# Optimization experiments

Hardware: AMD Instinct MI355X
Metric: run time of the kernel (lower is better)

Reference implementation:

```python
import jax, jax.numpy as jnp
import numpy as np

N_NODES = 100000


def gcn_conv(x, W, b, src, dst, n):
    # PyG GCNConv: linear transform, add self-loops, symmetric degree normalization,
    # scatter-add aggregation from src -> dst, then bias.
    h = x @ W  # [N, F_out]
    loop = jnp.arange(n, dtype=src.dtype)
    s = jnp.concatenate([src, loop])  # sources incl. self-loops
    d = jnp.concatenate([dst, loop])  # targets incl. self-loops
    deg = jax.ops.segment_sum(jnp.ones_like(d, dtype=h.dtype), d, num_segments=n)
    dinv = jnp.where(deg > 0, jax.lax.rsqrt(deg), 0.0)
    norm = dinv[s] * dinv[d]  # [E+N]
    msg = h[s] * norm[:, None]  # gather + scale
    out = jax.ops.segment_sum(msg, d, num_segments=n)  # scatter-add
    return out + b


def setup_inputs() -> dict:
    key = jax.random.key(0)
    k1, k2, k3, k4 = jax.random.split(key, 4)
    n, e = N_NODES, 1600000
    z = jax.random.normal(k1, (n, 64), dtype=jnp.float32)
    edge_index = jax.random.randint(k2, (2, e), 0, n, dtype=jnp.int64)
    # Glorot-ish init for weights, zero bias (PyG default bias init is zeros)
    W1 = jax.random.normal(k3, (64, 128), dtype=jnp.float32) * (1.0 / np.sqrt(64))
    b1 = jnp.zeros((128,), dtype=jnp.float32)
    W2 = jax.random.normal(k4, (128, 64), dtype=jnp.float32) * (1.0 / np.sqrt(128))
    b2 = jnp.zeros((64,), dtype=jnp.float32)
    return {"z": z, "edge_index": edge_index, "W1": W1, "b1": b1, "W2": W2, "b2": b2}


def reference(z, edge_index, W1, b1, W2, b2):
    n = z.shape[0]
    src, dst = edge_index[0], edge_index[1]
    h = gcn_conv(z, W1, b1, src, dst, n)
    h = jax.nn.relu(h)
    x_hat = gcn_conv(h, W2, b2, src, dst, n)
    return x_hat
```

## Files before the change

### kernel.cpp

```cpp
#include <hip/hip_runtime.h>
#include <hip/hip_bf16.h>


#define WAVE 64
#define BSHIFT 8
#define NPB 256
#define CAP 5120
#define CH 4096
#define NBMAX 512

__device__ inline float bf16_to_f32(unsigned short h) {
    return __uint_as_float(((unsigned int)h) << 16);
}
__device__ inline unsigned short f32_to_bf16(float f) {
    unsigned int x = __float_as_uint(f);
    return (unsigned short)((x + 0x7FFFu + ((x >> 16) & 1u)) >> 16);
}

__global__ void zero_i32(int* __restrict__ p, int n) {
    int i = blockIdx.x * blockDim.x + threadIdx.x;
    if (i < n) p[i] = 0;
}

__global__ __launch_bounds__(256) void bin_edges(
        const int* __restrict__ src, const int* __restrict__ dst,
        int* __restrict__ bcursor, int2* __restrict__ ebuf, int E, int NB)
{
    __shared__ int hist[NBMAX];
    __shared__ int cur[NBMAX];
    const int t  = threadIdx.x;
    const int e0 = blockIdx.x * CH;

    for (int b = t; b < NB; b += 256) hist[b] = 0;
    __syncthreads();

#pragma unroll
    for (int j = 0; j < CH / 256; ++j) {
        int e = e0 + j * 256 + t;
        if (e < E) atomicAdd(&hist[dst[e] >> BSHIFT], 1);
    }
    __syncthreads();

    for (int b = t; b < NB; b += 256) {
        int c = hist[b];
        cur[b] = (c > 0) ? atomicAdd(&bcursor[b], c) : 0;
    }
    __syncthreads();

#pragma unroll
    for (int j = 0; j < CH / 256; ++j) {
        int e = e0 + j * 256 + t;
        if (e < E) {
            int s = src[e], d = dst[e];
            int b = d >> BSHIFT;
            int pos = atomicAdd(&cur[b], 1);
            ebuf[(size_t)b * CAP + pos] = make_int2(s, d);
        }
    }
}

__global__ __launch_bounds__(256) void build_csr(
        const int2* __restrict__ ebuf, const int* __restrict__ bcursor,
        const float* __restrict__ z, float* __restrict__ dinv,
        int* __restrict__ rbeg, int* __restrict__ rend,
        int* __restrict__ csr, unsigned short* __restrict__ u, int N)
{
    __shared__ int   h[NPB];
    __shared__ int   tmp[NPB];
    __shared__ float sdv[NPB];
    const int t   = threadIdx.x;
    const int b   = blockIdx.x;
    const int n0  = b << BSHIFT;
    const int cnt = bcursor[b];
    const size_t base = (size_t)b * CAP;

    h[t] = 0;
    __syncthreads();

    for (int i = t; i < cnt; i += 256)
        atomicAdd(&h[ebuf[base + i].y - n0], 1);
    __syncthreads();

    int deg = h[t];
    tmp[t] = deg;
    __syncthreads();
    for (int off = 1; off < 256; off <<= 1) {
        int x = (t >= off) ? tmp[t - off] : 0;
        __syncthreads();
        tmp[t] += x;
        __syncthreads();
    }
    int st = tmp[t] - deg;

    int node = n0 + t;
    float di = rsqrtf((float)deg + 1.0f);
    sdv[t] = di;
    if (node < N) {
        dinv[node] = di;
        rbeg[node] = (int)base + st;
        rend[node] = (int)base + st + deg;
    }
    h[t] = st;
    __syncthreads();

    for (int i = t; i < cnt; i += 256) {
        int2 e = ebuf[base + i];
        int p = atomicAdd(&h[e.y - n0], 1);
        csr[base + p] = e.x;
    }

    const int nloc = (N - n0 < NPB) ? (N - n0) : NPB;
    for (int i = t; i < nloc * 16; i += 256) {
        int r = i >> 4, kq = i & 15;
        float d2 = sdv[r];
        float4 v = ((const float4*)(z + (size_t)(n0 + r) * 64))[kq];
        ushort4 o;
        o.x = f32_to_bf16(v.x * d2);
        o.y = f32_to_bf16(v.y * d2);
        o.z = f32_to_bf16(v.z * d2);
        o.w = f32_to_bf16(v.w * d2);
        ((ushort4*)(u + (size_t)(n0 + r) * 64))[kq] = o;
    }
}

template<bool POST>
__global__ __launch_bounds__(256) void aggregate64_bf16(
        const unsigned short* __restrict__ hs, const int* __restrict__ rbeg,
        const int* __restrict__ rend, const int* __restrict__ csr,
        const float* __restrict__ dinv, const float* __restrict__ b,
        float* __restrict__ out, int N)
{
    int node = (int)((blockIdx.x * (size_t)blockDim.x + threadIdx.x) >> 6);
    int lane = threadIdx.x & 63;
    if (node >= N) return;
    node = __builtin_amdgcn_readfirstlane(node);

    const int beg = rbeg[node];
    const int end = rend[node];

    float acc = bf16_to_f32(hs[(size_t)node * 64 + lane]);

    int e = beg;
    for (; e + 16 <= end; e += 16) {
        int s[16];
#pragma unroll
        for (int j = 0; j < 16; ++j) s[j] = csr[e + j];
        float v[16];
#pragma unroll
        for (int j = 0; j < 16; ++j) v[j] = bf16_to_f32(hs[(size_t)s[j] * 64 + lane]);
        float t0 = ((v[0] + v[1]) + (v[2] + v[3])) + ((v[4] + v[5]) + (v[6] + v[7]));
        float t1 = ((v[8] + v[9]) + (v[10] + v[11])) + ((v[12] + v[13]) + (v[14] + v[15]));
        acc += t0 + t1;
    }
    for (; e + 4 <= end; e += 4) {
        int s0 = csr[e+0], s1 = csr[e+1], s2 = csr[e+2], s3 = csr[e+3];
        float v0 = bf16_to_f32(hs[(size_t)s0 * 64 + lane]);
        float v1 = bf16_to_f32(hs[(size_t)s1 * 64 + lane]);
        float v2 = bf16_to_f32(hs[(size_t)s2 * 64 + lane]);
        float v3 = bf16_to_f32(hs[(size_t)s3 * 64 + lane]);
        acc += (v0 + v1) + (v2 + v3);
    }
    for (; e < end; ++e)
        acc += bf16_to_f32(hs[(size_t)csr[e] * 64 + lane]);

    float o = acc;
    if (POST) o = dinv[node] * acc + b[lane];
    out[(size_t)node * 64 + lane] = o;
}

#define TILE 32
__global__ __launch_bounds__(256) void gemm12(
        const float* __restrict__ agg1, const float* __restrict__ W1,
        const float* __restrict__ b1, const float* __restrict__ W2,
        const float* __restrict__ dinv, unsigned short* __restrict__ hs2, int N)
{
    __shared__ float4 Wl[2048];
    __shared__ float4 Al[TILE * 17];
    __shared__ float4 X1[TILE * 33];
    __shared__ float  sdv[TILE];

    const int tid  = threadIdx.x;
    const int row0 = blockIdx.x * TILE;

#pragma unroll
    for (int i = tid; i < 2048; i += 256) Wl[i] = ((const float4*)W1)[i];
    for (int i = tid; i < TILE * 16; i += 256) {
        int r = i >> 4, kq = i & 15;
        int gr = row0 + r;
        float4 v = make_float4(0.f, 0.f, 0.f, 0.f);
        if (gr < N) v = ((const float4*)(agg1 + (size_t)gr * 64))[kq];
        Al[r * 17 + kq] = v;
    }
    if (tid < TILE) {
        int gr = row0 + tid;
        sdv[tid] = (gr < N) ? dinv[gr] : 0.0f;
    }
    __syncthreads();

    {
        constexpr int C4 = 32, G = 8, RPT = TILE / G;
        const int c4 = tid % C4;
        const int rg = tid / C4;
        float4 acc[RPT];
#pragma unroll
        for (int r = 0; r < RPT; ++r) acc[r] = make_float4(0.f, 0.f, 0.f, 0.f);

#pragma unroll 2
        for (int kq = 0; kq < 16; ++kq) {
            float4 w0 = Wl[(4 * kq + 0) * C4 + c4];
            float4 w1 = Wl[(4 * kq + 1) * C4 + c4];
            float4 w2 = Wl[(4 * kq + 2) * C4 + c4];
            float4 w3 = Wl[(4 * kq + 3) * C4 + c4];
#pragma unroll
            for (int r = 0; r < RPT; ++r) {
                float4 a = Al[(rg * RPT + r) * 17 + kq];
                acc[r].x += a.x * w0.x; acc[r].y += a.x * w0.y;
                acc[r].z += a.x * w0.z; acc[r].w += a.x * w0.w;
                acc[r].x += a.y * w1.x; acc[r].y += a.y * w1.y;
                acc[r].z += a.y * w1.z; acc[r].w += a.y * w1.w;
                acc[r].x += a.z * w2.x; acc[r].y += a.z * w2.y;
                acc[r].z += a.z * w2.z; acc[r].w += a.z * w2.w;
                acc[r].x += a.w * w3.x; acc[r].y += a.w * w3.y;
                acc[r].z += a.w * w3.z; acc[r].w += a.w * w3.w;
            }
        }

        float4 bb = ((const float4*)b1)[c4];
#pragma unroll
        for (int r = 0; r < RPT; ++r) {
            int lr = rg * RPT + r;
            float di = sdv[lr];
            float4 o = acc[r];
            o.x = fmaxf(o.x * di + bb.x, 0.0f);
            o.y = fmaxf(o.y * di + bb.y, 0.0f);
            o.z = fmaxf(o.z * di + bb.z, 0.0f);
            o.w = fmaxf(o.w * di + bb.w, 0.0f);
            X1[lr * 33 + c4] = o;
        }
    }
    __syncthreads();

#pragma unroll
    for (int i = tid; i < 2048; i += 256) Wl[i] = ((const float4*)W2)[i];
    __syncthreads();

    {
        constexpr int C4 = 16, G = 16, RPT = TILE / G;
        const int c4 = tid % C4;
        const int rg = tid / C4;
        float4 acc[RPT];
#pragma unroll
        for (int r = 0; r < RPT; ++r) acc[r] = make_float4(0.f, 0.f, 0.f, 0.f);

#pragma unroll 2
        for (int kq = 0; kq < 32; ++kq) {
            float4 w0 = Wl[(4 * kq + 0) * C4 + c4];
            float4 w1 = Wl[(4 * kq + 1) * C4 + c4];
            float4 w2 = Wl[(4 * kq + 2) * C4 + c4];
            float4 w3 = Wl[(4 * kq + 3) * C4 + c4];
#pragma unroll
            for (int r = 0; r < RPT; ++r) {
                float4 a = X1[(rg * RPT + r) * 33 + kq];
                acc[r].x += a.x * w0.x; acc[r].y += a.x * w0.y;
                acc[r].z += a.x * w0.z; acc[r].w += a.x * w0.w;
                acc[r].x += a.y * w1.x; acc[r].y += a.y * w1.y;
                acc[r].z += a.y * w1.z; acc[r].w += a.y * w1.w;
                acc[r].x += a.z * w2.x; acc[r].y += a.z * w2.y;
                acc[r].z += a.z * w2.z; acc[r].w += a.z * w2.w;
                acc[r].x += a.w * w3.x; acc[r].y += a.w * w3.y;
                acc[r].z += a.w * w3.z; acc[r].w += a.w * w3.w;
            }
        }

#pragma unroll
        for (int r = 0; r < RPT; ++r) {
            int lr = rg * RPT + r;
            int gr = row0 + lr;
            if (gr < N) {
                float di = sdv[lr];
                float4 o = acc[r];
                ushort4 ob;
                ob.x = f32_to_bf16(o.x * di);
                ob.y = f32_to_bf16(o.y * di);
                ob.z = f32_to_bf16(o.z * di);
                ob.w = f32_to_bf16(o.w * di);
                ((ushort4*)(hs2 + (size_t)gr * 64))[c4] = ob;
            }
        }
    }
}

static inline size_t align_up(size_t x, size_t a) { return (x + a - 1) / a * a; }

extern "C" void kernel_launch(void* const* d_in, const int* in_sizes, int n_in,
                              void* d_out, int out_size, void* d_ws, size_t ws_size,
                              hipStream_t stream) {
    const float* z    = (const float*)d_in[0];
    const int*   eidx = (const int*)d_in[1];
    const float* W1   = (const float*)d_in[2];
    const float* b1   = (const float*)d_in[3];
    const float* W2   = (const float*)d_in[4];
    const float* b2   = (const float*)d_in[5];
    float* out = (float*)d_out;

    const int N = in_sizes[0] / 64;
    const int E = in_sizes[1] / 2;
    const int* src = eidx;
    const int* dst = eidx + E;
    const int NB = (N + NPB - 1) >> BSHIFT;

    char* ws = (char*)d_ws;
    size_t off = 0;
    float* dinv    = (float*)(ws + off); off = align_up(off + (size_t)N * 4, 512);
    int*   rbeg    = (int*)  (ws + off); off = align_up(off + (size_t)N * 4, 512);
    int*   rend    = (int*)  (ws + off); off = align_up(off + (size_t)N * 4, 512);
    int*   bcursor = (int*)  (ws + off); off = align_up(off + (size_t)NBMAX * 4, 512);
    int*   csr     = (int*)  (ws + off); off = align_up(off + (size_t)NB * CAP * 4, 512);
    float* bufA    = (float*)(ws + off); off = align_up(off + (size_t)N * 64 * 4, 512);
    float* bufB    = (float*)(ws + off); off = align_up(off + (size_t)N * 64 * 4, 512);
    float* bufC    = (float*)(ws + off); off = align_up(off + (size_t)N * 128 * 4, 512);
    int2*  ebuf    = (int2*)bufC;
    (void)ws_size;

    unsigned short* u    = (unsigned short*)bufA;
    float*          agg1 = bufB;
    unsigned short* hs2  = (unsigned short*)bufA;

    zero_i32<<<(NB + 255) / 256, 256, 0, stream>>>(bcursor, NB);
    bin_edges<<<(E + CH - 1) / CH, 256, 0, stream>>>(src, dst, bcursor, ebuf, E, NB);
    build_csr<<<NB, 256, 0, stream>>>(ebuf, bcursor, z, dinv, rbeg, rend, csr, u, N);

    aggregate64_bf16<false><<<(N + 3) / 4, 256, 0, stream>>>(u, rbeg, rend, csr, dinv, nullptr, agg1, N);

    gemm12<<<(N + TILE - 1) / TILE, 256, 0, stream>>>(agg1, W1, b1, W2, dinv, hs2, N);

    aggregate64_bf16<true><<<(N + 3) / 4, 256, 0, stream>>>(hs2, rbeg, rend, csr, dinv, b2, out, N);
}
```

Measured before the change: 276.4 us.

## Use bf16 MFMA for fused two-layer GEMM and store first aggregation in bf16

Replaces the FP32 FMA-based fused GEMM with MFMA bf16 16x16x32 instructions. The weights are pre-transposed to bf16 in a prep kernel, which also takes over zeroing the bin cursors. The first aggregation now writes its output as bf16, halving the intermediate store and the GEMM's read traffic. The aim is to cut GEMM compute time and memory bandwidth, at the cost of extra bf16 rounding of the aggregated features and the hidden activations.

```diff
diff --git a/kernel.cpp b/kernel.cpp
--- a/kernel.cpp
+++ b/kernel.cpp
@@ -9,6 +9,9 @@
 #define CH 4096
 #define NBMAX 512
 
+typedef __attribute__((ext_vector_type(8))) short bf16x8;
+typedef __attribute__((ext_vector_type(4))) float f32x4;
+
 __device__ inline float bf16_to_f32(unsigned short h) {
     return __uint_as_float(((unsigned int)h) << 16);
 }
@@ -17,9 +20,20 @@
     return (unsigned short)((x + 0x7FFFu + ((x >> 16) & 1u)) >> 16);
 }
 
-__global__ void zero_i32(int* __restrict__ p, int n) {
+__global__ void prep(const float* __restrict__ W1, const float* __restrict__ W2,
+                     unsigned short* __restrict__ W1t, unsigned short* __restrict__ W2t,
+                     int* __restrict__ bcursor, int NB)
+{
     int i = blockIdx.x * blockDim.x + threadIdx.x;
-    if (i < n) p[i] = 0;
+    if (i < NB) bcursor[i] = 0;
+    if (i < 128 * 64) {
+        int n = i >> 6, k = i & 63;
+        W1t[i] = f32_to_bf16(W1[k * 128 + n]);
+    }
+    if (i < 64 * 128) {
+        int n = i >> 7, k = i & 127;
+        W2t[i] = f32_to_bf16(W2[k * 64 + n]);
+    }
 }
 
 __global__ __launch_bounds__(256) void bin_edges(
@@ -128,7 +142,7 @@
         const unsigned short* __restrict__ hs, const int* __restrict__ rbeg,
         const int* __restrict__ rend, const int* __restrict__ csr,
         const float* __restrict__ dinv, const float* __restrict__ b,
-        float* __restrict__ out, int N)
+        void* __restrict__ out_, int N)
 {
     int node = (int)((blockIdx.x * (size_t)blockDim.x + threadIdx.x) >> 6);
     int lane = threadIdx.x & 63;
@@ -163,33 +177,55 @@
     for (; e < end; ++e)
         acc += bf16_to_f32(hs[(size_t)csr[e] * 64 + lane]);
 
-    float o = acc;
-    if (POST) o = dinv[node] * acc + b[lane];
-    out[(size_t)node * 64 + lane] = o;
+    if (POST) {
+        float o = dinv[node] * acc + b[lane];
+        ((float*)out_)[(size_t)node * 64 + lane] = o;
+    } else {
+        ((unsigned short*)out_)[(size_t)node * 64 + lane] = f32_to_bf16(acc);
+    }
 }
 
 #define TILE 32
-__global__ __launch_bounds__(256) void gemm12(
-        const float* __restrict__ agg1, const float* __restrict__ W1,
-        const float* __restrict__ b1, const float* __restrict__ W2,
-        const float* __restrict__ dinv, unsigned short* __restrict__ hs2, int N)
-{
-    __shared__ float4 Wl[2048];
-    __shared__ float4 Al[TILE * 17];
-    __shared__ float4 X1[TILE * 33];
-    __shared__ float  sdv[TILE];
+#define W1T_ST 72
+#define W2T_ST 136
+#define A_ST   72
+#define X1_ST  136
+
+__global__ __launch_bounds__(256) void gemm12_mfma(
+        const unsigned short* __restrict__ agg1,
+        const unsigned short* __restrict__ W1t,
+        const float* __restrict__ b1,
+        const unsigned short* __restrict__ W2t,
+        const float* __restrict__ dinv,
+        unsigned short* __restrict__ hs2, int N)
+{
+    __shared__ unsigned short sW1[128 * W1T_ST];
+    __shared__ unsigned short sW2[64 * W2T_ST];
+    __shared__ unsigned short sA[TILE * A_ST];
+    __shared__ unsigned short sX[TILE * X1_ST];
+    __shared__ float sdv[TILE];
 
     const int tid  = threadIdx.x;
     const int row0 = blockIdx.x * TILE;
-
-#pragma unroll
-    for (int i = tid; i < 2048; i += 256) Wl[i] = ((const float4*)W1)[i];
-    for (int i = tid; i < TILE * 16; i += 256) {
-        int r = i >> 4, kq = i & 15;
+    const int lane = tid & 63;
+    const int wv   = tid >> 6;
+    const int l16  = lane & 15;
+    const int quad = lane >> 4;
+
+    for (int i = tid; i < 128 * 8; i += 256) {
+        int r = i >> 3, c = i & 7;
+        *(uint4*)&sW1[r * W1T_ST + c * 8] = *(const uint4*)&W1t[r * 64 + c * 8];
+    }
+    for (int i = tid; i < 64 * 16; i += 256) {
+        int r = i >> 4, c = i & 15;
+        *(uint4*)&sW2[r * W2T_ST + c * 8] = *(const uint4*)&W2t[r * 128 + c * 8];
+    }
+    for (int i = tid; i < TILE * 8; i += 256) {
+        int r = i >> 3, c = i & 7;
         int gr = row0 + r;
-        float4 v = make_float4(0.f, 0.f, 0.f, 0.f);
-        if (gr < N) v = ((const float4*)(agg1 + (size_t)gr * 64))[kq];
-        Al[r * 17 + kq] = v;
+        uint4 v = make_uint4(0u, 0u, 0u, 0u);
+        if (gr < N) v = *(const uint4*)&agg1[(size_t)gr * 64 + c * 8];
+        *(uint4*)&sA[r * A_ST + c * 8] = v;
     }
     if (tid < TILE) {
         int gr = row0 + tid;
@@ -198,93 +234,62 @@
     __syncthreads();
 
     {
-        constexpr int C4 = 32, G = 8, RPT = TILE / G;
-        const int c4 = tid % C4;
-        const int rg = tid / C4;
-        float4 acc[RPT];
-#pragma unroll
-        for (int r = 0; r < RPT; ++r) acc[r] = make_float4(0.f, 0.f, 0.f, 0.f);
-
-#pragma unroll 2
-        for (int kq = 0; kq < 16; ++kq) {
-            float4 w0 = Wl[(4 * kq + 0) * C4 + c4];
-            float4 w1 = Wl[(4 * kq + 1) * C4 + c4];
-            float4 w2 = Wl[(4 * kq + 2) * C4 + c4];
-            float4 w3 = Wl[(4 * kq + 3) * C4 + c4];
-#pragma unroll
-            for (int r = 0; r < RPT; ++r) {
-                float4 a = Al[(rg * RPT + r) * 17 + kq];
-                acc[r].x += a.x * w0.x; acc[r].y += a.x * w0.y;
-                acc[r].z += a.x * w0.z; acc[r].w += a.x * w0.w;
-                acc[r].x += a.y * w1.x; acc[r].y += a.y * w1.y;
-                acc[r].z += a.y * w1.z; acc[r].w += a.y * w1.w;
-                acc[r].x += a.z * w2.x; acc[r].y += a.z * w2.y;
-                acc[r].z += a.z * w2.z; acc[r].w += a.z * w2.w;
-                acc[r].x += a.w * w3.x; acc[r].y += a.w * w3.y;
-                acc[r].z += a.w * w3.z; acc[r].w += a.w * w3.w;
+        const int mt  = wv & 1;
+        const int ntb = (wv >> 1) * 4;
+        f32x4 acc[4];
+#pragma unroll
+        for (int t = 0; t < 4; ++t) acc[t] = (f32x4)0.0f;
+
+#pragma unroll
+        for (int k0 = 0; k0 < 64; k0 += 32) {
+            bf16x8 af = *(const bf16x8*)&sA[(mt * 16 + l16) * A_ST + k0 + quad * 8];
+#pragma unroll
+            for (int t = 0; t < 4; ++t) {
+                bf16x8 bf = *(const bf16x8*)&sW1[((ntb + t) * 16 + l16) * W1T_ST + k0 + quad * 8];
+                acc[t] = __builtin_amdgcn_mfma_f32_16x16x32_bf16(af, bf, acc[t], 0, 0, 0);
             }
         }
 
-        float4 bb = ((const float4*)b1)[c4];
-#pragma unroll
-        for (int r = 0; r < RPT; ++r) {
-            int lr = rg * RPT + r;
-            float di = sdv[lr];
-            float4 o = acc[r];
-            o.x = fmaxf(o.x * di + bb.x, 0.0f);
-            o.y = fmaxf(o.y * di + bb.y, 0.0f);
-            o.z = fmaxf(o.z * di + bb.z, 0.0f);
-            o.w = fmaxf(o.w * di + bb.w, 0.0f);
-            X1[lr * 33 + c4] = o;
-        }
-    }
-    __syncthreads();
-
-#pragma unroll
-    for (int i = tid; i < 2048; i += 256) Wl[i] = ((const float4*)W2)[i];
+#pragma unroll
+        for (int t = 0; t < 4; ++t) {
+            int col = (ntb + t) * 16 + l16;
+            float bb = b1[col];
+#pragma unroll
+            for (int r = 0; r < 4; ++r) {
+                int lr = mt * 16 + quad * 4 + r;
+                float o = fmaxf(acc[t][r] * sdv[lr] + bb, 0.0f);
+                sX[lr * X1_ST + col] = f32_to_bf16(o);
+            }
+        }
+    }
     __syncthreads();
 
     {
-        constexpr int C4 = 16, G = 16, RPT = TILE / G;
-        const int c4 = tid % C4;
-        const int rg = tid / C4;
-        float4 acc[RPT];
-#pragma unroll
-        for (int r = 0; r < RPT; ++r) acc[r] = make_float4(0.f, 0.f, 0.f, 0.f);
-
-#pragma unroll 2
-        for (int kq = 0; kq < 32; ++kq) {
-            float4 w0 = Wl[(4 * kq + 0) * C4 + c4];
-            float4 w1 = Wl[(4 * kq + 1) * C4 + c4];
-            float4 w2 = Wl[(4 * kq + 2) * C4 + c4];
-            float4 w3 = Wl[(4 * kq + 3) * C4 + c4];
-#pragma unroll
-            for (int r = 0; r < RPT; ++r) {
-                float4 a = X1[(rg * RPT + r) * 33 + kq];
-                acc[r].x += a.x * w0.x; acc[r].y += a.x * w0.y;
-                acc[r].z += a.x * w0.z; acc[r].w += a.x * w0.w;
-                acc[r].x += a.y * w1.x; acc[r].y += a.y * w1.y;
-                acc[r].z += a.y * w1.z; acc[r].w += a.y * w1.w;
-                acc[r].x += a.z * w2.x; acc[r].y += a.z * w2.y;
-                acc[r].z += a.z * w2.z; acc[r].w += a.z * w2.w;
-                acc[r].x += a.w * w3.x; acc[r].y += a.w * w3.y;
-                acc[r].z += a.w * w3.z; acc[r].w += a.w * w3.w;
+        const int mt  = wv & 1;
+        const int ntb = (wv >> 1) * 2;
+        f32x4 acc[2];
+#pragma unroll
+        for (int t = 0; t < 2; ++t) acc[t] = (f32x4)0.0f;
+
+#pragma unroll
+        for (int k0 = 0; k0 < 128; k0 += 32) {
+            bf16x8 af = *(const bf16x8*)&sX[(mt * 16 + l16) * X1_ST + k0 + quad * 8];
+#pragma unroll
+            for (int t = 0; t < 2; ++t) {
+                bf16x8 bf = *(const bf16x8*)&sW2[((ntb + t) * 16 + l16) * W2T_ST + k0 + quad * 8];
+                acc[t] = __builtin_amdgcn_mfma_f32_16x16x32_bf16(af, bf, acc[t], 0, 0, 0);
             }
         }
 
 #pragma unroll
-        for (int r = 0; r < RPT; ++r) {
-            int lr = rg * RPT + r;
-            int gr = row0 + lr;
-            if (gr < N) {
-                float di = sdv[lr];
-                float4 o = acc[r];
-                ushort4 ob;
-                ob.x = f32_to_bf16(o.x * di);
-                ob.y = f32_to_bf16(o.y * di);
-                ob.z = f32_to_bf16(o.z * di);
-                ob.w = f32_to_bf16(o.w * di);
-                ((ushort4*)(hs2 + (size_t)gr * 64))[c4] = ob;
+        for (int t = 0; t < 2; ++t) {
+            int col = (ntb + t) * 16 + l16;
+#pragma unroll
+            for (int r = 0; r < 4; ++r) {
+                int lr = mt * 16 + quad * 4 + r;
+                int gr = row0 + lr;
+                if (gr < N)
+                    hs2[(size_t)gr * 64 + col] = f32_to_bf16(acc[t][r] * sdv[lr]);
             }
         }
     }
@@ -315,6 +320,8 @@
     int*   rbeg    = (int*)  (ws + off); off = align_up(off + (size_t)N * 4, 512);
     int*   rend    = (int*)  (ws + off); off = align_up(off + (size_t)N * 4, 512);
     int*   bcursor = (int*)  (ws + off); off = align_up(off + (size_t)NBMAX * 4, 512);
+    unsigned short* W1t = (unsigned short*)(ws + off); off = align_up(off + 8192 * 2, 512);
+    unsigned short* W2t = (unsigned short*)(ws + off); off = align_up(off + 8192 * 2, 512);
     int*   csr     = (int*)  (ws + off); off = align_up(off + (size_t)NB * CAP * 4, 512);
     float* bufA    = (float*)(ws + off); off = align_up(off + (size_t)N * 64 * 4, 512);
     float* bufB    = (float*)(ws + off); off = align_up(off + (size_t)N * 64 * 4, 512);
@@ -323,16 +330,17 @@
     (void)ws_size;
 
     unsigned short* u    = (unsigned short*)bufA;
-    float*          agg1 = bufB;
+    unsigned short* agg1 = (unsigned short*)bufB;
     unsigned short* hs2  = (unsigned short*)bufA;
 
-    zero_i32<<<(NB + 255) / 256, 256, 0, stream>>>(bcursor, NB);
+    prep<<<32, 256, 0, stream>>>(W1, W2, W1t, W2t, bcursor, NB);
+
     bin_edges<<<(E + CH - 1) / CH, 256, 0, stream>>>(src, dst, bcursor, ebuf, E, NB);
     build_csr<<<NB, 256, 0, stream>>>(ebuf, bcursor, z, dinv, rbeg, rend, csr, u, N);
 
     aggregate64_bf16<false><<<(N + 3) / 4, 256, 0, stream>>>(u, rbeg, rend, csr, dinv, nullptr, agg1, N);
 
-    gemm12<<<(N + TILE - 1) / TILE, 256, 0, stream>>>(agg1, W1, b1, W2, dinv, hs2, N);
+    gemm12_mfma<<<(N + TILE - 1) / TILE, 256, 0, stream>>>(agg1, W1t, b1, W2t, dinv, hs2, N);
 
     aggregate64_bf16<true><<<(N + 3) / 4, 256, 0, stream>>>(hs2, rbeg, rend, csr, dinv, b2, out, N);
 }
```

Measured after the change: 237.3 us. 14.1% less time.
